# Performance work log

Hardware: AMD Instinct MI355X
Metric: run time of the kernel (lower is better)

## Reference

```python
import jax, jax.numpy as jnp
import numpy as np

T, C, H = 2048, 1024, 16
D = C // H  # head dim = 64


def setup_inputs() -> dict:
    key = jax.random.key(0)
    k1, k2, k3 = jax.random.split(key, 3)
    x = jax.random.normal(k1, (T, C), dtype=jnp.float32)
    W_qkv = jax.random.normal(k2, (C, 3 * C), dtype=jnp.float32) * (1.0 / np.sqrt(C))
    b_qkv = jnp.zeros((3 * C,), dtype=jnp.float32)
    W_proj = jax.random.normal(k3, (C, C), dtype=jnp.float32) * (1.0 / np.sqrt(C))
    b_proj = jnp.zeros((C,), dtype=jnp.float32)
    return {"x": x, "W_qkv": W_qkv, "b_qkv": b_qkv, "W_proj": W_proj, "b_proj": b_proj}


def reference(x, W_qkv, b_qkv, W_proj, b_proj):
    t, c = x.shape
    qkv = x @ W_qkv + b_qkv                      # [T, 3C] fused QKV projection
    q, k, v = jnp.split(qkv, 3, axis=-1)         # each [T, C]
    # split heads: [T, C] -> [H, T, D]
    q = q.reshape(t, H, D).transpose(1, 0, 2)
    k = k.reshape(t, H, D).transpose(1, 0, 2)
    v = v.reshape(t, H, D).transpose(1, 0, 2)
    # naive O(T^2) attention, full score matrix [H, T, T]
    att = jnp.einsum('htd,hsd->hts', q, k) / jnp.sqrt(jnp.float32(D))
    att = jax.nn.softmax(att, axis=-1)
    y = jnp.einsum('hts,hsd->htd', att, v)       # [H, T, D]
    y = y.transpose(1, 0, 2).reshape(t, c)       # merge heads -> [T, C]
    return y @ W_proj + b_proj
```

## Files before the change

### kernel.cpp

```cpp
#include <hip/hip_runtime.h>
#include <hip/hip_bf16.h>
#include <stdint.h>

#define T_DIM 2048
#define C_DIM 1024
#define H_DIM 16
#define D_HEAD 64
#define N_QKV 3072
#define CQ 0.18033688011112042f

typedef __bf16 bf16;
typedef __bf16 bf16x8 __attribute__((ext_vector_type(8)));
typedef __bf16 bf16x4 __attribute__((ext_vector_type(4)));
typedef __bf16 bf16x2 __attribute__((ext_vector_type(2)));
typedef float f32x4 __attribute__((ext_vector_type(4)));
typedef short s16x4 __attribute__((ext_vector_type(4)));

__device__ __forceinline__ void lds_load16(const void* g, void* l) {
    __builtin_amdgcn_global_load_lds(
        (const __attribute__((address_space(1))) void*)g,
        (__attribute__((address_space(3))) void*)l, 16, 0, 0);
}

__device__ __forceinline__ f32x4 mfma16(bf16x4 a, bf16x4 b, f32x4 c) {
#if __has_builtin(__builtin_amdgcn_mfma_f32_16x16x16_bf16)
    return __builtin_amdgcn_mfma_f32_16x16x16_bf16(a, b, c, 0, 0, 0);
#elif __has_builtin(__builtin_amdgcn_mfma_f32_16x16x16bf16_1k)
    union { bf16x4 v; s16x4 s; } ua, ub;
    ua.v = a; ub.v = b;
    return __builtin_amdgcn_mfma_f32_16x16x16bf16_1k(ua.s, ub.s, c, 0, 0, 0);
#else
    asm volatile("v_mfma_f32_16x16x16_bf16 %0, %1, %2, %0"
                 : "+v"(c) : "v"(a), "v"(b));
    return c;
#endif
}

__global__ void prep_kernel(const float* __restrict__ x, bf16* __restrict__ xb,
                            const float* __restrict__ Wq, bf16* __restrict__ WqT,
                            const float* __restrict__ Wp, bf16* __restrict__ WpT) {
    __shared__ float tile[32][33];
    int bid = blockIdx.x;
    int t = threadIdx.x;
    if (bid < 1024) {
        int i = (bid * 256 + t) * 8;
        float4 a = *(const float4*)(x + i);
        float4 b = *(const float4*)(x + i + 4);
        bf16x8 o;
        o[0] = (bf16)a.x; o[1] = (bf16)a.y; o[2] = (bf16)a.z; o[3] = (bf16)a.w;
        o[4] = (bf16)b.x; o[5] = (bf16)b.y; o[6] = (bf16)b.z; o[7] = (bf16)b.w;
        *(bf16x8*)(xb + i) = o;
        return;
    }
    bid -= 1024;
    const float* in; bf16* out; int N, nb, kb;
    if (bid < 3072) { in = Wq; out = WqT; N = N_QKV; nb = (bid % 96) * 32; kb = (bid / 96) * 32; }
    else { bid -= 3072; in = Wp; out = WpT; N = C_DIM; nb = (bid % 32) * 32; kb = (bid / 32) * 32; }
    int r = t >> 3, c4 = (t & 7) * 4;
    float4 v = *(const float4*)(in + (size_t)(kb + r) * N + nb + c4);
    tile[r][c4 + 0] = v.x; tile[r][c4 + 1] = v.y;
    tile[r][c4 + 2] = v.z; tile[r][c4 + 3] = v.w;
    __syncthreads();
    bf16x4 ov;
    ov[0] = (bf16)tile[c4 + 0][r]; ov[1] = (bf16)tile[c4 + 1][r];
    ov[2] = (bf16)tile[c4 + 2][r]; ov[3] = (bf16)tile[c4 + 3][r];
    *(bf16x4*)(out + (size_t)(nb + r) * C_DIM + kb + c4) = ov;
}

#define QKV_STAGE(BUF, K0) do {                                                      \
    lds_load16(ga + (K0),                            &As[BUF][0][(w * 16) * 32]);    \
    lds_load16(ga + (K0) + 32,                       &As[BUF][1][(w * 16) * 32]);    \
    lds_load16(ga + (size_t)64 * C_DIM + (K0),       &As[BUF][0][(64 + w * 16) * 32]); \
    lds_load16(ga + (size_t)64 * C_DIM + (K0) + 32,  &As[BUF][1][(64 + w * 16) * 32]); \
    lds_load16(gb + (K0),                            &Bs[BUF][0][(w * 16) * 32]);    \
    lds_load16(gb + (K0) + 32,                       &Bs[BUF][1][(w * 16) * 32]);    \
    lds_load16(gb + (size_t)64 * C_DIM + (K0),       &Bs[BUF][0][(64 + w * 16) * 32]); \
    lds_load16(gb + (size_t)64 * C_DIM + (K0) + 32,  &Bs[BUF][1][(64 + w * 16) * 32]); \
} while (0)

#define QKV_COMPUTE(BUF) do {                                                \
    _Pragma("unroll")                                                        \
    for (int p = 0; p < 2; ++p) {                                            \
        bf16x8 af[4], bfr[4];                                                \
        _Pragma("unroll")                                                    \
        for (int mi = 0; mi < 4; ++mi) af[mi]  = *(const bf16x8*)&As[BUF][p][(wm + mi * 16 + lo16) * 32 + quad * 8]; \
        _Pragma("unroll")                                                    \
        for (int ni = 0; ni < 4; ++ni) bfr[ni] = *(const bf16x8*)&Bs[BUF][p][(wn + ni * 16 + lo16) * 32 + quad * 8]; \
        _Pragma("unroll")                                                    \
        for (int mi = 0; mi < 4; ++mi)                                       \
            _Pragma("unroll")                                                \
            for (int ni = 0; ni < 4; ++ni)                                   \
                acc[mi][ni] = __builtin_amdgcn_mfma_f32_16x16x32_bf16(af[mi], bfr[ni], acc[mi][ni], 0, 0, 0); \
    }                                                                        \
} while (0)

#define WAIT_AND_BARRIER() do {                                              \
    asm volatile("s_waitcnt vmcnt(0)" ::: "memory");                         \
    __builtin_amdgcn_s_barrier();                                            \
} while (0)

__global__ __launch_bounds__(256, 2) void qkv_gemm_kernel(
    const bf16* __restrict__ A, const bf16* __restrict__ Bt,
    const float* __restrict__ bias, bf16* __restrict__ qkv)
{
    __shared__ __align__(16) bf16 As[2][2][128 * 32];
    __shared__ __align__(16) bf16 Bs[2][2][128 * 32];
    const int bid = blockIdx.x;
    const int xcd = bid & 7, slot = bid >> 3;
    const int rowBase = (slot / 3) * 128;
    const int colBase = (xcd * 3 + (slot % 3)) * 128;
    const int tid = threadIdx.x, lane = tid & 63, w = tid >> 6;
    const int lo16 = lane & 15, quad = lane >> 4;
    const int wm = (w & 1) * 64, wn = (w >> 1) * 64;

    const bf16* ga = A  + (size_t)(rowBase + w * 16 + (lane >> 2)) * C_DIM + (lane & 3) * 8;
    const bf16* gb = Bt + (size_t)(colBase + w * 16 + (lane >> 2)) * C_DIM + (lane & 3) * 8;

    f32x4 acc[4][4] = {};

    QKV_STAGE(0, 0);
    WAIT_AND_BARRIER();

    for (int k0 = 0; k0 < C_DIM; k0 += 128) {
        QKV_STAGE(1, k0 + 64);
        QKV_COMPUTE(0);
        WAIT_AND_BARRIER();
        if (k0 + 128 < C_DIM) QKV_STAGE(0, k0 + 128);
        QKV_COMPUTE(1);
        WAIT_AND_BARRIER();
    }

    const float scale = (colBase < C_DIM) ? CQ : 1.0f;
    #pragma unroll
    for (int ni = 0; ni < 4; ++ni) {
        int col = colBase + wn + ni * 16 + lo16;
        float bv = bias[col];
        #pragma unroll
        for (int mi = 0; mi < 4; ++mi) {
            int row0 = rowBase + wm + mi * 16 + quad * 4;
            #pragma unroll
            for (int r = 0; r < 4; ++r)
                qkv[(size_t)(row0 + r) * N_QKV + col] = (bf16)((acc[mi][ni][r] + bv) * scale);
        }
    }
}

__global__ __launch_bounds__(512, 2) void flash_kernel(
    const bf16* __restrict__ qkv,
    bf16* __restrict__ y)
{
    __shared__ union {
        __align__(16) bf16 Vt[4][64][38];
        float Ored[8][16][66];
    } u;
    __shared__ float lred[8][64];

    const int bid = blockIdx.x;
    const int xcd = bid & 7, slot = bid >> 3;
    const int h = xcd * 2 + (slot & 1);
    const int qb = slot >> 1;
    const int tid  = threadIdx.x;
    const int lane = tid & 63, w = tid >> 6;
    const int lo16 = lane & 15, quad = lane >> 4;

    bf16x8 qf[4][2];
    #pragma unroll
    for (int nq = 0; nq < 4; ++nq)
        #pragma unroll
        for (int dk = 0; dk < 2; ++dk)
            qf[nq][dk] = *(const bf16x8*)(qkv + (size_t)(qb * 64 + nq * 16 + lo16) * N_QKV
                                          + h * D_HEAD + dk * 32 + quad * 8);

    f32x4 o_t[4][4] = {};
    f32x4 o_l[4] = {};
    bf16x4 ones1;
    ones1[0] = (bf16)1.0f; ones1[1] = (bf16)1.0f; ones1[2] = (bf16)1.0f; ones1[3] = (bf16)1.0f;

    const bf16* kfb = qkv + (size_t)(w * 16 + lo16) * N_QKV + C_DIM + h * D_HEAD + quad * 8;
    const unsigned short* vb16 = (const unsigned short*)(qkv + 2 * C_DIM + h * D_HEAD);

    bf16x8 kf0 = *(const bf16x8*)(kfb);
    bf16x8 kf1 = *(const bf16x8*)(kfb + 32);
    unsigned short vreg[16];
    #pragma unroll
    for (int i = 0; i < 16; ++i)
        vreg[i] = vb16[(size_t)(w * 16 + i) * N_QKV + lane];

    bf16* vdst = &u.Vt[w >> 1][lane][(w & 1) * 16];

    for (int kt = 0; kt < T_DIM / 128; ++kt) {
        union { bf16x8 v; unsigned short us[8]; } p0, p1;
        #pragma unroll
        for (int i = 0; i < 8; ++i) { p0.us[i] = vreg[i]; p1.us[i] = vreg[8 + i]; }
        *(bf16x8*)vdst       = p0.v;
        *(bf16x8*)(vdst + 8) = p1.v;

        bf16x4 vf[4];
        #pragma unroll
        for (int mi = 0; mi < 4; ++mi)
            vf[mi] = *(const bf16x4*)&u.Vt[w >> 1][mi * 16 + lo16][(w & 1) * 16 + quad * 4];

        bf16x8 nkf0 = kf0, nkf1 = kf1;
        if (kt + 1 < T_DIM / 128) {
            const bf16* kp = kfb + (size_t)(kt + 1) * 128 * N_QKV;
            nkf0 = *(const bf16x8*)(kp);
            nkf1 = *(const bf16x8*)(kp + 32);
            #pragma unroll
            for (int i = 0; i < 16; ++i)
                vreg[i] = vb16[(size_t)((kt + 1) * 128 + w * 16 + i) * N_QKV + lane];
        }

        f32x4 st[4];
        #pragma unroll
        for (int nq = 0; nq < 4; ++nq) {
            f32x4 z = {};
            z = __builtin_amdgcn_mfma_f32_16x16x32_bf16(kf0, qf[nq][0], z, 0, 0, 0);
            st[nq] = __builtin_amdgcn_mfma_f32_16x16x32_bf16(kf1, qf[nq][1], z, 0, 0, 0);
        }

        bf16x4 pb[4];
        #pragma unroll
        for (int nq = 0; nq < 4; ++nq)
            #pragma unroll
            for (int r = 0; r < 4; ++r)
                pb[nq][r] = (bf16)__builtin_amdgcn_exp2f(st[nq][r]);

        __builtin_amdgcn_s_setprio(1);
        #pragma unroll
        for (int nq = 0; nq < 4; ++nq)
            o_l[nq] = mfma16(ones1, pb[nq], o_l[nq]);
        #pragma unroll
        for (int mi = 0; mi < 4; ++mi)
            #pragma unroll
            for (int nq = 0; nq < 4; ++nq)
                o_t[mi][nq] = mfma16(vf[mi], pb[nq], o_t[mi][nq]);
        __builtin_amdgcn_s_setprio(0);

        kf0 = nkf0; kf1 = nkf1;
    }

    #pragma unroll
    for (int nq = 0; nq < 4; ++nq)
        if (quad == 0) lred[w][nq * 16 + lo16] = o_l[nq][0];

    const int q8 = tid >> 3, dh = tid & 7;
    float linv = 0.f;
    #pragma unroll
    for (int mi = 0; mi < 4; ++mi) {
        __syncthreads();
        #pragma unroll
        for (int nq = 0; nq < 4; ++nq)
            #pragma unroll
            for (int r = 0; r < 4; ++r)
                u.Ored[w][quad * 4 + r][nq * 16 + lo16] = o_t[mi][nq][r];
        __syncthreads();
        if (mi == 0) {
            float ls = 0.f;
            #pragma unroll
            for (int j = 0; j < 8; ++j) ls += lred[j][q8];
            linv = 1.0f / ls;
        }
        bf16x2 ov;
        #pragma unroll
        for (int dj = 0; dj < 2; ++dj) {
            int d = dh * 2 + dj;
            float s = 0.f;
            #pragma unroll
            for (int j = 0; j < 8; ++j) s += u.Ored[j][d][q8];
            ov[dj] = (bf16)(s * linv);
        }
        *(bf16x2*)&y[(size_t)(qb * 64 + q8) * C_DIM + h * D_HEAD + mi * 16 + dh * 2] = ov;
    }
}

#define PROJ_STAGE(BUF, K0) do {                                             \
    lds_load16(ga + (K0),      &As[BUF][0][(w * 16) * 32]);                  \
    lds_load16(ga + (K0) + 32, &As[BUF][1][(w * 16) * 32]);                  \
    lds_load16(gb + (K0),      &Bs[BUF][0][(w * 16) * 32]);                  \
    lds_load16(gb + (K0) + 32, &Bs[BUF][1][(w * 16) * 32]);                  \
} while (0)

#define PROJ_COMPUTE(BUF) do {                                               \
    _Pragma("unroll")                                                        \
    for (int p = 0; p < 2; ++p) {                                            \
        bf16x8 af[2], bfr[2];                                                \
        _Pragma("unroll")                                                    \
        for (int mi = 0; mi < 2; ++mi) af[mi]  = *(const bf16x8*)&As[BUF][p][(wm + mi * 16 + lo16) * 32 + quad * 8]; \
        _Pragma("unroll")                                                    \
        for (int ni = 0; ni < 2; ++ni) bfr[ni] = *(const bf16x8*)&Bs[BUF][p][(wn + ni * 16 + lo16) * 32 + quad * 8]; \
        _Pragma("unroll")                                                    \
        for (int mi = 0; mi < 2; ++mi)                                       \
            _Pragma("unroll")                                                \
            for (int ni = 0; ni < 2; ++ni)                                   \
                acc[mi][ni] = __builtin_amdgcn_mfma_f32_16x16x32_bf16(af[mi], bfr[ni], acc[mi][ni], 0, 0, 0); \
    }                                                                        \
} while (0)

__global__ __launch_bounds__(256, 4) void proj_gemm_kernel(
    const bf16* __restrict__ A, const bf16* __restrict__ Bt,
    const float* __restrict__ bias, float* __restrict__ out)
{
    __shared__ __align__(16) bf16 As[2][2][64 * 32];
    __shared__ __align__(16) bf16 Bs[2][2][64 * 32];
    const int bid = blockIdx.x;
    const int xcd = bid & 7, slot = bid >> 3;
    const int colBase = (xcd * 2 + (slot & 1)) * 64;
    const int rowBase = (slot >> 1) * 64;
    const int tid = threadIdx.x, lane = tid & 63, w = tid >> 6;
    const int lo16 = lane & 15, quad = lane >> 4;
    const int wm = (w & 1) * 32, wn = (w >> 1) * 32;

    const bf16* ga = A  + (size_t)(rowBase + w * 16 + (lane >> 2)) * C_DIM + (lane & 3) * 8;
    const bf16* gb = Bt + (size_t)(colBase + w * 16 + (lane >> 2)) * C_DIM + (lane & 3) * 8;

    f32x4 acc[2][2] = {};

    PROJ_STAGE(0, 0);
    WAIT_AND_BARRIER();

    for (int k0 = 0; k0 < C_DIM; k0 += 128) {
        PROJ_STAGE(1, k0 + 64);
        PROJ_COMPUTE(0);
        WAIT_AND_BARRIER();
        if (k0 + 128 < C_DIM) PROJ_STAGE(0, k0 + 128);
        PROJ_COMPUTE(1);
        WAIT_AND_BARRIER();
    }

    #pragma unroll
    for (int ni = 0; ni < 2; ++ni) {
        int col = colBase + wn + ni * 16 + lo16;
        float bv = bias[col];
        #pragma unroll
        for (int mi = 0; mi < 2; ++mi) {
            int row0 = rowBase + wm + mi * 16 + quad * 4;
            #pragma unroll
            for (int r = 0; r < 4; ++r)
                out[(size_t)(row0 + r) * C_DIM + col] = acc[mi][ni][r] + bv;
        }
    }
}

extern "C" void kernel_launch(void* const* d_in, const int* in_sizes, int n_in,
                              void* d_out, int out_size, void* d_ws, size_t ws_size,
                              hipStream_t stream) {
    const float* x      = (const float*)d_in[0];
    const float* W_qkv  = (const float*)d_in[1];
    const float* b_qkv  = (const float*)d_in[2];
    const float* W_proj = (const float*)d_in[3];
    const float* b_proj = (const float*)d_in[4];
    float* out = (float*)d_out;

    char* ws = (char*)d_ws;
    bf16* xb      = (bf16*)(ws);
    bf16* Wqkv_t  = (bf16*)(ws + (4  << 20));
    bf16* Wproj_t = (bf16*)(ws + (10 << 20));
    bf16* qkv_bf  = (bf16*)(ws + (12 << 20));
    bf16* yb      = (bf16*)(ws + (24 << 20));

    prep_kernel<<<5120, 256, 0, stream>>>(x, xb, W_qkv, Wqkv_t, W_proj, Wproj_t);

    qkv_gemm_kernel<<<384, 256, 0, stream>>>(xb, Wqkv_t, b_qkv, qkv_bf);

    flash_kernel<<<512, 512, 0, stream>>>(qkv_bf, yb);

    proj_gemm_kernel<<<512, 256, 0, stream>>>(yb, Wproj_t, b_proj, out);
}
```

Measured before the change: 145.3 us.

## Load V fragments directly from global and drop LDS transpose in flash kernel

Swaps the operand order of the PV and row-sum MFMAs so V can be loaded straight from global memory in its natural row layout. This removes the per-iteration LDS transpose of V. The loop is manually unrolled by two with double-buffered V registers (vA/vB), and the score MFMAs get a priority boost. The output reduction is reorganised to match the transposed accumulator layout. The trade-off is that each lane now issues more scalar 2-byte global loads with strided access, instead of the previous LDS traffic.

```diff
diff --git a/kernel.cpp b/kernel.cpp
--- a/kernel.cpp
+++ b/kernel.cpp
@@ -145,14 +145,55 @@
     }
 }
 
+#define NKT (T_DIM / 128)
+
+#define FLASH_IT(KT, VC, VN)                                                          \
+    {                                                                                 \
+        bf16x8 nkf0 = kf0, nkf1 = kf1;                                                \
+        if ((KT) + 1 < NKT) {                                                         \
+            const bf16* kp = kfb + (size_t)((KT) + 1) * 128 * N_QKV;                  \
+            nkf0 = *(const bf16x8*)(kp);                                              \
+            nkf1 = *(const bf16x8*)(kp + 32);                                         \
+            const bf16* vp = vfb + (size_t)((KT) + 1) * 128 * N_QKV;                  \
+            _Pragma("unroll")                                                         \
+            for (int mi = 0; mi < 4; ++mi)                                            \
+                _Pragma("unroll")                                                     \
+                for (int i = 0; i < 4; ++i)                                           \
+                    VN[mi][i] = vp[(size_t)i * N_QKV + mi * 16];                      \
+        }                                                                             \
+        f32x4 st[4];                                                                  \
+        __builtin_amdgcn_s_setprio(1);                                                \
+        _Pragma("unroll")                                                             \
+        for (int nq = 0; nq < 4; ++nq) {                                              \
+            f32x4 z = {};                                                             \
+            z = __builtin_amdgcn_mfma_f32_16x16x32_bf16(kf0, qf[nq][0], z, 0, 0, 0);  \
+            st[nq] = __builtin_amdgcn_mfma_f32_16x16x32_bf16(kf1, qf[nq][1], z, 0, 0, 0); \
+        }                                                                             \
+        __builtin_amdgcn_s_setprio(0);                                                \
+        bf16x4 pb[4];                                                                 \
+        _Pragma("unroll")                                                             \
+        for (int nq = 0; nq < 4; ++nq)                                                \
+            _Pragma("unroll")                                                         \
+            for (int r = 0; r < 4; ++r)                                               \
+                pb[nq][r] = (bf16)__builtin_amdgcn_exp2f(st[nq][r]);                  \
+        __builtin_amdgcn_s_setprio(1);                                                \
+        _Pragma("unroll")                                                             \
+        for (int nq = 0; nq < 4; ++nq)                                                \
+            o_l[nq] = mfma16(pb[nq], ones1, o_l[nq]);                                 \
+        _Pragma("unroll")                                                             \
+        for (int nq = 0; nq < 4; ++nq)                                                \
+            _Pragma("unroll")                                                         \
+            for (int mi = 0; mi < 4; ++mi)                                            \
+                o_t[nq][mi] = mfma16(pb[nq], VC[mi], o_t[nq][mi]);                    \
+        __builtin_amdgcn_s_setprio(0);                                                \
+        kf0 = nkf0; kf1 = nkf1;                                                       \
+    }
+
 __global__ __launch_bounds__(512, 2) void flash_kernel(
     const bf16* __restrict__ qkv,
     bf16* __restrict__ y)
 {
-    __shared__ union {
-        __align__(16) bf16 Vt[4][64][38];
-        float Ored[8][16][66];
-    } u;
+    __shared__ float Ored[8][16][67];
     __shared__ float lred[8][64];
 
     const int bid = blockIdx.x;
@@ -177,99 +218,50 @@
     ones1[0] = (bf16)1.0f; ones1[1] = (bf16)1.0f; ones1[2] = (bf16)1.0f; ones1[3] = (bf16)1.0f;
 
     const bf16* kfb = qkv + (size_t)(w * 16 + lo16) * N_QKV + C_DIM + h * D_HEAD + quad * 8;
-    const unsigned short* vb16 = (const unsigned short*)(qkv + 2 * C_DIM + h * D_HEAD);
+    const bf16* vfb = qkv + (size_t)(w * 16 + quad * 4) * N_QKV + 2 * C_DIM + h * D_HEAD + lo16;
 
     bf16x8 kf0 = *(const bf16x8*)(kfb);
     bf16x8 kf1 = *(const bf16x8*)(kfb + 32);
-    unsigned short vreg[16];
+    bf16x4 vA[4], vB[4];
     #pragma unroll
-    for (int i = 0; i < 16; ++i)
-        vreg[i] = vb16[(size_t)(w * 16 + i) * N_QKV + lane];
-
-    bf16* vdst = &u.Vt[w >> 1][lane][(w & 1) * 16];
-
-    for (int kt = 0; kt < T_DIM / 128; ++kt) {
-        union { bf16x8 v; unsigned short us[8]; } p0, p1;
-        #pragma unroll
-        for (int i = 0; i < 8; ++i) { p0.us[i] = vreg[i]; p1.us[i] = vreg[8 + i]; }
-        *(bf16x8*)vdst       = p0.v;
-        *(bf16x8*)(vdst + 8) = p1.v;
-
-        bf16x4 vf[4];
-        #pragma unroll
-        for (int mi = 0; mi < 4; ++mi)
-            vf[mi] = *(const bf16x4*)&u.Vt[w >> 1][mi * 16 + lo16][(w & 1) * 16 + quad * 4];
-
-        bf16x8 nkf0 = kf0, nkf1 = kf1;
-        if (kt + 1 < T_DIM / 128) {
-            const bf16* kp = kfb + (size_t)(kt + 1) * 128 * N_QKV;
-            nkf0 = *(const bf16x8*)(kp);
-            nkf1 = *(const bf16x8*)(kp + 32);
-            #pragma unroll
-            for (int i = 0; i < 16; ++i)
-                vreg[i] = vb16[(size_t)((kt + 1) * 128 + w * 16 + i) * N_QKV + lane];
-        }
-
-        f32x4 st[4];
-        #pragma unroll
-        for (int nq = 0; nq < 4; ++nq) {
-            f32x4 z = {};
-            z = __builtin_amdgcn_mfma_f32_16x16x32_bf16(kf0, qf[nq][0], z, 0, 0, 0);
-            st[nq] = __builtin_amdgcn_mfma_f32_16x16x32_bf16(kf1, qf[nq][1], z, 0, 0, 0);
-        }
-
-        bf16x4 pb[4];
+    for (int mi = 0; mi < 4; ++mi)
+        #pragma unroll
+        for (int i = 0; i < 4; ++i)
+            vA[mi][i] = vfb[(size_t)i * N_QKV + mi * 16];
+
+    for (int kt = 0; kt < NKT; kt += 2) {
+        FLASH_IT(kt,     vA, vB);
+        FLASH_IT(kt + 1, vB, vA);
+    }
+
+    if (lo16 == 0) {
         #pragma unroll
         for (int nq = 0; nq < 4; ++nq)
             #pragma unroll
-            for (int r = 0; r < 4; ++r)
-                pb[nq][r] = (bf16)__builtin_amdgcn_exp2f(st[nq][r]);
-
-        __builtin_amdgcn_s_setprio(1);
-        #pragma unroll
-        for (int nq = 0; nq < 4; ++nq)
-            o_l[nq] = mfma16(ones1, pb[nq], o_l[nq]);
+            for (int i = 0; i < 4; ++i)
+                lred[w][nq * 16 + quad * 4 + i] = o_l[nq][i];
+    }
+
+    const int qloc = tid >> 5;
+    const int d0   = (tid & 31) * 2;
+    for (int nq = 0; nq < 4; ++nq) {
+        __syncthreads();
         #pragma unroll
         for (int mi = 0; mi < 4; ++mi)
             #pragma unroll
-            for (int nq = 0; nq < 4; ++nq)
-                o_t[mi][nq] = mfma16(vf[mi], pb[nq], o_t[mi][nq]);
-        __builtin_amdgcn_s_setprio(0);
-
-        kf0 = nkf0; kf1 = nkf1;
-    }
-
-    #pragma unroll
-    for (int nq = 0; nq < 4; ++nq)
-        if (quad == 0) lred[w][nq * 16 + lo16] = o_l[nq][0];
-
-    const int q8 = tid >> 3, dh = tid & 7;
-    float linv = 0.f;
-    #pragma unroll
-    for (int mi = 0; mi < 4; ++mi) {
+            for (int i = 0; i < 4; ++i)
+                Ored[w][quad * 4 + i][mi * 16 + lo16] = o_t[nq][mi][i];
         __syncthreads();
-        #pragma unroll
-        for (int nq = 0; nq < 4; ++nq)
-            #pragma unroll
-            for (int r = 0; r < 4; ++r)
-                u.Ored[w][quad * 4 + r][nq * 16 + lo16] = o_t[mi][nq][r];
-        __syncthreads();
-        if (mi == 0) {
-            float ls = 0.f;
-            #pragma unroll
-            for (int j = 0; j < 8; ++j) ls += lred[j][q8];
-            linv = 1.0f / ls;
-        }
+        float ls = 0.f;
+        #pragma unroll
+        for (int j = 0; j < 8; ++j) ls += lred[j][nq * 16 + qloc];
+        float linv = 1.0f / ls;
+        float s0 = 0.f, s1 = 0.f;
+        #pragma unroll
+        for (int j = 0; j < 8; ++j) { s0 += Ored[j][qloc][d0]; s1 += Ored[j][qloc][d0 + 1]; }
         bf16x2 ov;
-        #pragma unroll
-        for (int dj = 0; dj < 2; ++dj) {
-            int d = dh * 2 + dj;
-            float s = 0.f;
-            #pragma unroll
-            for (int j = 0; j < 8; ++j) s += u.Ored[j][d][q8];
-            ov[dj] = (bf16)(s * linv);
-        }
-        *(bf16x2*)&y[(size_t)(qb * 64 + q8) * C_DIM + h * D_HEAD + mi * 16 + dh * 2] = ov;
+        ov[0] = (bf16)(s0 * linv); ov[1] = (bf16)(s1 * linv);
+        *(bf16x2*)&y[(size_t)(qb * 64 + nq * 16 + qloc) * C_DIM + h * D_HEAD + d0] = ov;
     }
 }
 
```

Result: slower. 150.2 us (+3.3%).

## Restructure flash kernel: smaller blocks, async double-buffered V staging to LDS

Applied to the files above, without the earlier changes.

The attention kernel now uses 256-thread blocks, each covering 32 queries, with a 1024-block grid in place of 512 blocks of 512 threads covering 64 queries. V tiles of 64 keys are now staged with global_load_lds into double-buffered, XOR-swizzled shared memory. This replaces the old per-lane ushort gathers followed by a register transpose through LDS. The PV MFMA operand order and the final cross-wave reduction are reworked to match the new layout. The aim is higher occupancy, fewer scattered global loads and load latency hidden behind compute, at the cost of a barrier on every key tile and half as much K/V reuse per block.

```diff
diff --git a/kernel.cpp b/kernel.cpp
--- a/kernel.cpp
+++ b/kernel.cpp
@@ -145,15 +145,23 @@
     }
 }
 
-__global__ __launch_bounds__(512, 2) void flash_kernel(
+#define NKT (T_DIM / 64)
+
+#define STAGE_V(B, KT) do {                                                  \
+    const bf16* vs_ = vsrc + (size_t)(KT) * 64 * N_QKV;                      \
+    lds_load16(vs_,                         &u.Vs[(B) * 4096 + w * 512]);    \
+    lds_load16(vs_ + (size_t)32 * N_QKV,    &u.Vs[(B) * 4096 + 2048 + w * 512]); \
+} while (0)
+
+__global__ __launch_bounds__(256, 3) void flash_kernel(
     const bf16* __restrict__ qkv,
     bf16* __restrict__ y)
 {
     __shared__ union {
-        __align__(16) bf16 Vt[4][64][38];
-        float Ored[8][16][66];
+        __align__(16) bf16 Vs[2 * 4096];
+        float Ored[4][16][68];
     } u;
-    __shared__ float lred[8][64];
+    __shared__ float lred[4][32];
 
     const int bid = blockIdx.x;
     const int xcd = bid & 7, slot = bid >> 3;
@@ -163,113 +171,108 @@
     const int lane = tid & 63, w = tid >> 6;
     const int lo16 = lane & 15, quad = lane >> 4;
 
-    bf16x8 qf[4][2];
+    bf16x8 qf[2][2];
     #pragma unroll
-    for (int nq = 0; nq < 4; ++nq)
+    for (int nq = 0; nq < 2; ++nq)
         #pragma unroll
         for (int dk = 0; dk < 2; ++dk)
-            qf[nq][dk] = *(const bf16x8*)(qkv + (size_t)(qb * 64 + nq * 16 + lo16) * N_QKV
+            qf[nq][dk] = *(const bf16x8*)(qkv + (size_t)(qb * 32 + nq * 16 + lo16) * N_QKV
                                           + h * D_HEAD + dk * 32 + quad * 8);
 
-    f32x4 o_t[4][4] = {};
-    f32x4 o_l[4] = {};
+    f32x4 o_t[2][4] = {};
+    f32x4 o_l[2] = {};
     bf16x4 ones1;
     ones1[0] = (bf16)1.0f; ones1[1] = (bf16)1.0f; ones1[2] = (bf16)1.0f; ones1[3] = (bf16)1.0f;
 
     const bf16* kfb = qkv + (size_t)(w * 16 + lo16) * N_QKV + C_DIM + h * D_HEAD + quad * 8;
-    const unsigned short* vb16 = (const unsigned short*)(qkv + 2 * C_DIM + h * D_HEAD);
+    const int vcol = ((tid & 7) << 3) ^ (((tid >> 5) & 3) << 4);
+    const bf16* vsrc = qkv + 2 * C_DIM + h * D_HEAD + (size_t)(tid >> 3) * N_QKV + vcol;
+    const int vrbase = (w * 16 + quad * 4) * 64 + lo16;
 
     bf16x8 kf0 = *(const bf16x8*)(kfb);
     bf16x8 kf1 = *(const bf16x8*)(kfb + 32);
-    unsigned short vreg[16];
-    #pragma unroll
-    for (int i = 0; i < 16; ++i)
-        vreg[i] = vb16[(size_t)(w * 16 + i) * N_QKV + lane];
-
-    bf16* vdst = &u.Vt[w >> 1][lane][(w & 1) * 16];
-
-    for (int kt = 0; kt < T_DIM / 128; ++kt) {
-        union { bf16x8 v; unsigned short us[8]; } p0, p1;
-        #pragma unroll
-        for (int i = 0; i < 8; ++i) { p0.us[i] = vreg[i]; p1.us[i] = vreg[8 + i]; }
-        *(bf16x8*)vdst       = p0.v;
-        *(bf16x8*)(vdst + 8) = p1.v;
+    STAGE_V(0, 0);
+
+    for (int kt = 0; kt < NKT; ++kt) {
+        const int b = kt & 1;
+        WAIT_AND_BARRIER();
 
         bf16x4 vf[4];
         #pragma unroll
         for (int mi = 0; mi < 4; ++mi)
-            vf[mi] = *(const bf16x4*)&u.Vt[w >> 1][mi * 16 + lo16][(w & 1) * 16 + quad * 4];
+            #pragma unroll
+            for (int j = 0; j < 4; ++j)
+                vf[mi][j] = u.Vs[b * 4096 + vrbase + j * 64 + (((mi ^ quad)) << 4)];
 
         bf16x8 nkf0 = kf0, nkf1 = kf1;
-        if (kt + 1 < T_DIM / 128) {
-            const bf16* kp = kfb + (size_t)(kt + 1) * 128 * N_QKV;
+        if (kt + 1 < NKT) {
+            STAGE_V(b ^ 1, kt + 1);
+            const bf16* kp = kfb + (size_t)(kt + 1) * 64 * N_QKV;
             nkf0 = *(const bf16x8*)(kp);
             nkf1 = *(const bf16x8*)(kp + 32);
-            #pragma unroll
-            for (int i = 0; i < 16; ++i)
-                vreg[i] = vb16[(size_t)((kt + 1) * 128 + w * 16 + i) * N_QKV + lane];
-        }
-
-        f32x4 st[4];
-        #pragma unroll
-        for (int nq = 0; nq < 4; ++nq) {
+        }
+
+        f32x4 st[2];
+        __builtin_amdgcn_s_setprio(1);
+        #pragma unroll
+        for (int nq = 0; nq < 2; ++nq) {
             f32x4 z = {};
             z = __builtin_amdgcn_mfma_f32_16x16x32_bf16(kf0, qf[nq][0], z, 0, 0, 0);
             st[nq] = __builtin_amdgcn_mfma_f32_16x16x32_bf16(kf1, qf[nq][1], z, 0, 0, 0);
         }
-
-        bf16x4 pb[4];
-        #pragma unroll
-        for (int nq = 0; nq < 4; ++nq)
+        __builtin_amdgcn_s_setprio(0);
+
+        bf16x4 pb[2];
+        #pragma unroll
+        for (int nq = 0; nq < 2; ++nq)
             #pragma unroll
             for (int r = 0; r < 4; ++r)
                 pb[nq][r] = (bf16)__builtin_amdgcn_exp2f(st[nq][r]);
 
         __builtin_amdgcn_s_setprio(1);
         #pragma unroll
-        for (int nq = 0; nq < 4; ++nq)
+        for (int nq = 0; nq < 2; ++nq)
             o_l[nq] = mfma16(ones1, pb[nq], o_l[nq]);
         #pragma unroll
+        for (int nq = 0; nq < 2; ++nq)
+            #pragma unroll
+            for (int mi = 0; mi < 4; ++mi)
+                o_t[nq][mi] = mfma16(pb[nq], vf[mi], o_t[nq][mi]);
+        __builtin_amdgcn_s_setprio(0);
+
+        kf0 = nkf0; kf1 = nkf1;
+    }
+
+    if (quad == 0) {
+        #pragma unroll
+        for (int nq = 0; nq < 2; ++nq)
+            lred[w][nq * 16 + lo16] = o_l[nq][0];
+    }
+
+    const int qloc = tid >> 4;
+    const int d0   = (tid & 15) * 4;
+    #pragma unroll
+    for (int nq = 0; nq < 2; ++nq) {
+        __syncthreads();
+        #pragma unroll
         for (int mi = 0; mi < 4; ++mi)
             #pragma unroll
-            for (int nq = 0; nq < 4; ++nq)
-                o_t[mi][nq] = mfma16(vf[mi], pb[nq], o_t[mi][nq]);
-        __builtin_amdgcn_s_setprio(0);
-
-        kf0 = nkf0; kf1 = nkf1;
-    }
-
-    #pragma unroll
-    for (int nq = 0; nq < 4; ++nq)
-        if (quad == 0) lred[w][nq * 16 + lo16] = o_l[nq][0];
-
-    const int q8 = tid >> 3, dh = tid & 7;
-    float linv = 0.f;
-    #pragma unroll
-    for (int mi = 0; mi < 4; ++mi) {
+            for (int i = 0; i < 4; ++i)
+                u.Ored[w][quad * 4 + i][mi * 16 + lo16] = o_t[nq][mi][i];
         __syncthreads();
-        #pragma unroll
-        for (int nq = 0; nq < 4; ++nq)
-            #pragma unroll
-            for (int r = 0; r < 4; ++r)
-                u.Ored[w][quad * 4 + r][nq * 16 + lo16] = o_t[mi][nq][r];
-        __syncthreads();
-        if (mi == 0) {
-            float ls = 0.f;
-            #pragma unroll
-            for (int j = 0; j < 8; ++j) ls += lred[j][q8];
-            linv = 1.0f / ls;
-        }
-        bf16x2 ov;
-        #pragma unroll
-        for (int dj = 0; dj < 2; ++dj) {
-            int d = dh * 2 + dj;
+        float ls = 0.f;
+        #pragma unroll
+        for (int j = 0; j < 4; ++j) ls += lred[j][nq * 16 + qloc];
+        float linv = 1.0f / ls;
+        bf16x4 ov;
+        #pragma unroll
+        for (int di = 0; di < 4; ++di) {
             float s = 0.f;
             #pragma unroll
-            for (int j = 0; j < 8; ++j) s += u.Ored[j][d][q8];
-            ov[dj] = (bf16)(s * linv);
-        }
-        *(bf16x2*)&y[(size_t)(qb * 64 + q8) * C_DIM + h * D_HEAD + mi * 16 + dh * 2] = ov;
+            for (int j = 0; j < 4; ++j) s += u.Ored[j][qloc][d0 + di];
+            ov[di] = (bf16)(s * linv);
+        }
+        *(bf16x4*)&y[(size_t)(qb * 32 + nq * 16 + qloc) * C_DIM + h * D_HEAD + d0] = ov;
     }
 }
 
@@ -362,7 +365,7 @@
 
     qkv_gemm_kernel<<<384, 256, 0, stream>>>(xb, Wqkv_t, b_qkv, qkv_bf);
 
-    flash_kernel<<<512, 512, 0, stream>>>(qkv_bf, yb);
+    flash_kernel<<<1024, 256, 0, stream>>>(qkv_bf, yb);
 
     proj_gemm_kernel<<<512, 256, 0, stream>>>(yb, Wproj_t, b_proj, out);
 }
```

Measured after the change: 155.2 us. 6.8% more time.

## Software-pipeline attention loop and replace ones-MFMA row sums with VALU accumulation

Applied to the files above, without the earlier changes.

Restructures the key-tile loop so that the PV MFMAs for the previous tile are issued alongside the QK MFMAs of the current tile, with a prologue and epilogue, letting exp2 work overlap with matrix ops. The row-sum computation via an MFMA against a ones vector is replaced by a float accumulator updated during exp2, reduced at the end with cross-lane shuffles. This removes four MFMAs per tile and sums unrounded fp32 probabilities, at the cost of more live registers for the carried P and V fragments.

```diff
diff --git a/kernel.cpp b/kernel.cpp
--- a/kernel.cpp
+++ b/kernel.cpp
@@ -172,9 +172,7 @@
                                           + h * D_HEAD + dk * 32 + quad * 8);
 
     f32x4 o_t[4][4] = {};
-    f32x4 o_l[4] = {};
-    bf16x4 ones1;
-    ones1[0] = (bf16)1.0f; ones1[1] = (bf16)1.0f; ones1[2] = (bf16)1.0f; ones1[3] = (bf16)1.0f;
+    float l_acc[4] = {};
 
     const bf16* kfb = qkv + (size_t)(w * 16 + lo16) * N_QKV + C_DIM + h * D_HEAD + quad * 8;
     const unsigned short* vb16 = (const unsigned short*)(qkv + 2 * C_DIM + h * D_HEAD);
@@ -188,17 +186,62 @@
 
     bf16* vdst = &u.Vt[w >> 1][lane][(w & 1) * 16];
 
-    for (int kt = 0; kt < T_DIM / 128; ++kt) {
+    bf16x4 pbp[4];
+    bf16x4 vfp[4];
+
+    {
         union { bf16x8 v; unsigned short us[8]; } p0, p1;
         #pragma unroll
         for (int i = 0; i < 8; ++i) { p0.us[i] = vreg[i]; p1.us[i] = vreg[8 + i]; }
         *(bf16x8*)vdst       = p0.v;
         *(bf16x8*)(vdst + 8) = p1.v;
 
-        bf16x4 vf[4];
         #pragma unroll
         for (int mi = 0; mi < 4; ++mi)
-            vf[mi] = *(const bf16x4*)&u.Vt[w >> 1][mi * 16 + lo16][(w & 1) * 16 + quad * 4];
+            vfp[mi] = *(const bf16x4*)&u.Vt[w >> 1][mi * 16 + lo16][(w & 1) * 16 + quad * 4];
+
+        bf16x8 nkf0 = kf0, nkf1 = kf1;
+        {
+            const bf16* kp = kfb + (size_t)128 * N_QKV;
+            nkf0 = *(const bf16x8*)(kp);
+            nkf1 = *(const bf16x8*)(kp + 32);
+            #pragma unroll
+            for (int i = 0; i < 16; ++i)
+                vreg[i] = vb16[(size_t)(128 + w * 16 + i) * N_QKV + lane];
+        }
+
+        f32x4 st[4];
+        __builtin_amdgcn_s_setprio(1);
+        #pragma unroll
+        for (int nq = 0; nq < 4; ++nq) {
+            f32x4 z = {};
+            z = __builtin_amdgcn_mfma_f32_16x16x32_bf16(kf0, qf[nq][0], z, 0, 0, 0);
+            st[nq] = __builtin_amdgcn_mfma_f32_16x16x32_bf16(kf1, qf[nq][1], z, 0, 0, 0);
+        }
+        __builtin_amdgcn_s_setprio(0);
+
+        #pragma unroll
+        for (int nq = 0; nq < 4; ++nq)
+            #pragma unroll
+            for (int r = 0; r < 4; ++r) {
+                float p = __builtin_amdgcn_exp2f(st[nq][r]);
+                l_acc[nq] += p;
+                pbp[nq][r] = (bf16)p;
+            }
+        kf0 = nkf0; kf1 = nkf1;
+    }
+
+    for (int kt = 1; kt < T_DIM / 128; ++kt) {
+        union { bf16x8 v; unsigned short us[8]; } p0, p1;
+        #pragma unroll
+        for (int i = 0; i < 8; ++i) { p0.us[i] = vreg[i]; p1.us[i] = vreg[8 + i]; }
+        *(bf16x8*)vdst       = p0.v;
+        *(bf16x8*)(vdst + 8) = p1.v;
+
+        bf16x4 vfc[4];
+        #pragma unroll
+        for (int mi = 0; mi < 4; ++mi)
+            vfc[mi] = *(const bf16x4*)&u.Vt[w >> 1][mi * 16 + lo16][(w & 1) * 16 + quad * 4];
 
         bf16x8 nkf0 = kf0, nkf1 = kf1;
         if (kt + 1 < T_DIM / 128) {
@@ -211,37 +254,48 @@
         }
 
         f32x4 st[4];
+        __builtin_amdgcn_s_setprio(1);
         #pragma unroll
         for (int nq = 0; nq < 4; ++nq) {
             f32x4 z = {};
             z = __builtin_amdgcn_mfma_f32_16x16x32_bf16(kf0, qf[nq][0], z, 0, 0, 0);
             st[nq] = __builtin_amdgcn_mfma_f32_16x16x32_bf16(kf1, qf[nq][1], z, 0, 0, 0);
         }
-
-        bf16x4 pb[4];
+        #pragma unroll
+        for (int mi = 0; mi < 4; ++mi)
+            #pragma unroll
+            for (int nq = 0; nq < 4; ++nq)
+                o_t[mi][nq] = mfma16(vfp[mi], pbp[nq], o_t[mi][nq]);
+        __builtin_amdgcn_s_setprio(0);
+
         #pragma unroll
         for (int nq = 0; nq < 4; ++nq)
             #pragma unroll
-            for (int r = 0; r < 4; ++r)
-                pb[nq][r] = (bf16)__builtin_amdgcn_exp2f(st[nq][r]);
-
-        __builtin_amdgcn_s_setprio(1);
+            for (int r = 0; r < 4; ++r) {
+                float p = __builtin_amdgcn_exp2f(st[nq][r]);
+                l_acc[nq] += p;
+                pbp[nq][r] = (bf16)p;
+            }
+        #pragma unroll
+        for (int mi = 0; mi < 4; ++mi) vfp[mi] = vfc[mi];
+
+        kf0 = nkf0; kf1 = nkf1;
+    }
+
+    __builtin_amdgcn_s_setprio(1);
+    #pragma unroll
+    for (int mi = 0; mi < 4; ++mi)
         #pragma unroll
         for (int nq = 0; nq < 4; ++nq)
-            o_l[nq] = mfma16(ones1, pb[nq], o_l[nq]);
-        #pragma unroll
-        for (int mi = 0; mi < 4; ++mi)
-            #pragma unroll
-            for (int nq = 0; nq < 4; ++nq)
-                o_t[mi][nq] = mfma16(vf[mi], pb[nq], o_t[mi][nq]);
-        __builtin_amdgcn_s_setprio(0);
-
-        kf0 = nkf0; kf1 = nkf1;
-    }
-
-    #pragma unroll
-    for (int nq = 0; nq < 4; ++nq)
-        if (quad == 0) lred[w][nq * 16 + lo16] = o_l[nq][0];
+            o_t[mi][nq] = mfma16(vfp[mi], pbp[nq], o_t[mi][nq]);
+    __builtin_amdgcn_s_setprio(0);
+
+    #pragma unroll
+    for (int nq = 0; nq < 4; ++nq) {
+        l_acc[nq] += __shfl_xor(l_acc[nq], 16);
+        l_acc[nq] += __shfl_xor(l_acc[nq], 32);
+        if (quad == 0) lred[w][nq * 16 + lo16] = l_acc[nq];
+    }
 
     const int q8 = tid >> 3, dh = tid & 7;
     float linv = 0.f;
```

Result: no change. 146.9 us (+1.1%).
